# Kernel tuning notes

Measured on AMD Instinct MI355X. Metric: run time of the kernel, lower is better.

The kernel has to match this reference:

```python
import jax, jax.numpy as jnp
import numpy as np

N_NODES = 200000


def _gcn_conv(x, W, b, src, dst, n):
    # PyG GCNConv: h = D^{-1/2} (A + I) D^{-1/2} (x @ W) + b
    h = x @ W  # [N, F_out]
    deg = jax.ops.segment_sum(jnp.ones(dst.shape[0], x.dtype), dst, num_segments=n)
    dinv = jnp.where(deg > 0, jax.lax.rsqrt(deg), 0.0)  # deg_inv_sqrt, inf -> 0
    norm = dinv[src] * dinv[dst]  # [E+N]
    msg = h[src] * norm[:, None]  # gather + scale, dominant memory traffic
    out = jax.ops.segment_sum(msg, dst, num_segments=n)
    return out + b


def setup_inputs() -> dict:
    key = jax.random.key(0)
    k1, k2, k3, k4, k5, k6 = jax.random.split(key, 6)
    x = jax.random.normal(k1, (N_NODES, 1), dtype=jnp.float32)
    edge_index = jax.random.randint(k2, (2, 12800000), 0, N_NODES, dtype=jnp.int64)
    # Glorot-style init like PyG GCNConv
    W1 = jax.random.normal(k3, (1, 16), dtype=jnp.float32) * (1.0 / np.sqrt(1))
    b1 = jnp.zeros((16,), dtype=jnp.float32)
    W2 = jax.random.normal(k4, (16, 1), dtype=jnp.float32) * (1.0 / np.sqrt(16))
    b2 = jnp.zeros((1,), dtype=jnp.float32)
    return {"x": x, "edge_index": edge_index, "W1": W1, "b1": b1, "W2": W2, "b2": b2}


def reference(x, edge_index, W1, b1, W2, b2):
    n = x.shape[0]
    # add self-loops once (static edge count: E + N)
    loops = jnp.arange(n, dtype=edge_index.dtype)
    src = jnp.concatenate([edge_index[0], loops])
    dst = jnp.concatenate([edge_index[1], loops])
    h = _gcn_conv(x, W1, b1, src, dst, n)
    h = jax.nn.relu(h)
    out = _gcn_conv(h, W2, b2, src, dst, n)
    return out
```

## Files before the change

kernel.cpp:

```cpp
#include <hip/hip_runtime.h>

#define TPB 256
#define BTPB 1024
#define STPB 512
#define LOG_S 13
#define S (1 << LOG_S)
#define RMAX 32
#define CHUNK 8192
#define MAXC 40
#define SLACK 32768
#define SCALEF 2097152.0f
#define INV_SCALEF (1.0f / 2097152.0f)


__global__ void k_initcur(int* __restrict__ cur, int R, int cap) {
    int t = threadIdx.x;
    if (t < R) cur[t] = t * cap;
}

__global__ __launch_bounds__(BTPB) void k_bin(const int* __restrict__ dst,
                                              const int* __restrict__ src, int e,
                                              int R, int cap,
                                              int* __restrict__ cur,
                                              unsigned* __restrict__ bkt) {
    __shared__ unsigned stage[CHUNK];
    __shared__ int h[RMAX], lofs[RMAX + 1], gbase[RMAX];
    int t = threadIdx.x;
    int b0 = blockIdx.x * CHUNK;
    int m = min(CHUNK, e - b0);
    if (t < RMAX) h[t] = 0;
    __syncthreads();
    unsigned pack[8];
    int rr[8];
    const int4* d4p = (const int4*)(dst + b0);
    const int4* s4p = (const int4*)(src + b0);
    int m4 = m >> 2;
    #pragma unroll
    for (int g = 0; g < 2; g++) {
        int i4 = g * BTPB + t;
        if (i4 < m4) {
            int4 d = d4p[i4];
            int4 s = s4p[i4];
            #pragma unroll
            for (int k = 0; k < 4; k++) {
                int dd = (k == 0) ? d.x : (k == 1) ? d.y : (k == 2) ? d.z : d.w;
                int ss = (k == 0) ? s.x : (k == 1) ? s.y : (k == 2) ? s.z : s.w;
                int r = dd >> LOG_S;
                pack[g * 4 + k] = ((unsigned)(dd - (r << LOG_S)) << 18) | (unsigned)ss;
                int rk = atomicAdd(&h[r], 1);
                rr[g * 4 + k] = (r << 13) | rk;
            }
        } else {
            #pragma unroll
            for (int k = 0; k < 4; k++) rr[g * 4 + k] = -1;
        }
    }
    __syncthreads();
    if (t < 64) {
        int hv = (t < R) ? h[t] : 0;
        int v = hv;
        for (int o = 1; o < 64; o <<= 1) {
            int u = __shfl_up(v, o);
            if (t >= o) v += u;
        }
        if (t < R) lofs[t] = v - hv;
        if (t == R - 1) lofs[R] = v;
        if (t < R && hv > 0) gbase[t] = atomicAdd(&cur[t], hv);
    }
    __syncthreads();
    #pragma unroll
    for (int k = 0; k < 8; k++) {
        if (rr[k] >= 0)
            stage[lofs[rr[k] >> 13] + (rr[k] & 8191)] = pack[k];
    }
    __syncthreads();
    for (int j = t; j < m; j += BTPB) {
        int lo = 0, hi = R;
        while (hi - lo > 1) {
            int mid = (lo + hi) >> 1;
            if (lofs[mid] <= j) lo = mid; else hi = mid;
        }
        int gi = gbase[lo] + (j - lofs[lo]);
        if (gi < (lo + 1) * cap)
            bkt[gi] = stage[j];
    }
}

template <int MODE>
__global__ __launch_bounds__(STPB) void k_scat(const unsigned* __restrict__ bkt,
                                               const int* __restrict__ cur,
                                               int cap,
                                               const float* __restrict__ val,
                                               int* __restrict__ partials, int bpr) {
    __shared__ int acc[S];
    int t = threadIdx.x;
    int r = blockIdx.x / bpr;
    int c = blockIdx.x - r * bpr;
    int4* acc4 = (int4*)acc;
    for (int j = t; j < S / 4; j += STPB) acc4[j] = make_int4(0, 0, 0, 0);
    __syncthreads();
    const unsigned* bk = bkt + (size_t)r * cap;
    int len = min(cur[r] - r * cap, cap);
    int len4 = len >> 2;
    const uint4* bk4 = (const uint4*)bk;
    int stride = bpr * STPB;
    int i = c * STPB + t;
    if (i < len4) {
        uint4 p = bk4[i];
        for (;;) {
            int inext = i + stride;
            uint4 pn;
            bool hn = inext < len4;
            if (hn) pn = bk4[inext];
            if (MODE == 0) {
                atomicAdd(&acc[p.x >> 18], 1);
                atomicAdd(&acc[p.y >> 18], 1);
                atomicAdd(&acc[p.z >> 18], 1);
                atomicAdd(&acc[p.w >> 18], 1);
            } else {
                atomicAdd(&acc[p.x >> 18], (int)rintf(val[p.x & 0x3FFFFu] * SCALEF));
                atomicAdd(&acc[p.y >> 18], (int)rintf(val[p.y & 0x3FFFFu] * SCALEF));
                atomicAdd(&acc[p.z >> 18], (int)rintf(val[p.z & 0x3FFFFu] * SCALEF));
                atomicAdd(&acc[p.w >> 18], (int)rintf(val[p.w & 0x3FFFFu] * SCALEF));
            }
            if (!hn) break;
            p = pn;
            i = inext;
        }
    }
    for (int k = (len4 << 2) + c * STPB + t; k < len; k += stride) {
        unsigned p = bk[k];
        if (MODE == 0) atomicAdd(&acc[p >> 18], 1);
        else atomicAdd(&acc[p >> 18], (int)rintf(val[p & 0x3FFFFu] * SCALEF));
    }
    __syncthreads();
    int4* out4 = (int4*)(partials + (size_t)blockIdx.x * S);
    for (int j = t; j < S / 4; j += STPB) out4[j] = acc4[j];
}

__device__ inline int redp(const int* __restrict__ partials, int i, int bpr) {
    int r = i >> LOG_S;
    int slot = i & (S - 1);
    const int* p = partials + (size_t)r * bpr * S + slot;
    int s = 0;
    #pragma unroll 8
    for (int c = 0; c < bpr; c++) s += p[(size_t)c * S];
    return s;
}

__global__ void k_red_dinv(const int* __restrict__ partials, int bpr,
                           const float* __restrict__ x, float* __restrict__ dinv,
                           float* __restrict__ y, int n) {
    int i = blockIdx.x * blockDim.x + threadIdx.x;
    if (i < n) {
        float deg = (float)redp(partials, i, bpr) + 1.0f;
        float d = rsqrtf(deg);
        dinv[i] = d;
        y[i] = x[i] * d;
    }
}

__global__ void k_red_node(const int* __restrict__ partials, int bpr,
                           const float* __restrict__ dinv, const float* __restrict__ y,
                           float* __restrict__ z,
                           const float* __restrict__ W1, const float* __restrict__ b1,
                           const float* __restrict__ W2, int n, int f) {
    int i = blockIdx.x * blockDim.x + threadIdx.x;
    if (i < n) {
        float num = (float)redp(partials, i, bpr) * INV_SCALEF;
        float agg = dinv[i] * (num + y[i]);
        float h2 = 0.0f;
        for (int j = 0; j < f; j++) {
            float h = W1[j] * agg + b1[j];
            h2 += fmaxf(h, 0.0f) * W2[j];
        }
        z[i] = h2 * dinv[i];
    }
}

__global__ void k_red_out(const int* __restrict__ partials, int bpr,
                          const float* __restrict__ dinv, const float* __restrict__ z,
                          const float* __restrict__ b2, float* __restrict__ out, int n) {
    int i = blockIdx.x * blockDim.x + threadIdx.x;
    if (i < n) {
        float num = (float)redp(partials, i, bpr) * INV_SCALEF;
        out[i] = dinv[i] * (num + z[i]) + b2[0];
    }
}

__global__ void g_init(float* __restrict__ deg, float* __restrict__ num, int n) {
    int i = blockIdx.x * blockDim.x + threadIdx.x;
    if (i < n) { deg[i] = 1.0f; num[i] = 0.0f; }
}
__global__ void g_deg(const int* __restrict__ dst, float* __restrict__ deg, int e) {
    int i = blockIdx.x * blockDim.x + threadIdx.x;
    if (i < e) atomicAdd(deg + dst[i], 1.0f);
}
__global__ void g_dinv(const float* __restrict__ x, float* __restrict__ dd,
                       float* __restrict__ y, int n) {
    int i = blockIdx.x * blockDim.x + threadIdx.x;
    if (i < n) { float d = rsqrtf(dd[i]); dd[i] = d; y[i] = x[i] * d; }
}
__global__ void g_scatter(const int* __restrict__ src, const int* __restrict__ dst,
                          const float* __restrict__ val, float* __restrict__ num, int e) {
    int i = blockIdx.x * blockDim.x + threadIdx.x;
    if (i < e) atomicAdd(num + dst[i], val[src[i]]);
}
__global__ void g_node(const float* __restrict__ dinv, const float* __restrict__ y,
                       float* __restrict__ num, float* __restrict__ z,
                       const float* __restrict__ W1, const float* __restrict__ b1,
                       const float* __restrict__ W2, int n, int f) {
    int i = blockIdx.x * blockDim.x + threadIdx.x;
    if (i < n) {
        float agg = dinv[i] * (num[i] + y[i]);
        float h2 = 0.0f;
        for (int j = 0; j < f; j++) {
            float h = W1[j] * agg + b1[j];
            h2 += fmaxf(h, 0.0f) * W2[j];
        }
        z[i] = h2 * dinv[i];
        num[i] = 0.0f;
    }
}
__global__ void g_out(const float* __restrict__ dinv, const float* __restrict__ z,
                      const float* __restrict__ num, const float* __restrict__ b2,
                      float* __restrict__ out, int n) {
    int i = blockIdx.x * blockDim.x + threadIdx.x;
    if (i < n) out[i] = dinv[i] * (num[i] + z[i]) + b2[0];
}

extern "C" void kernel_launch(void* const* d_in, const int* in_sizes, int n_in,
                              void* d_out, int out_size, void* d_ws, size_t ws_size,
                              hipStream_t stream) {
    const float* x  = (const float*)d_in[0];
    const int*   ei = (const int*)d_in[1];
    const float* W1 = (const float*)d_in[2];
    const float* b1 = (const float*)d_in[3];
    const float* W2 = (const float*)d_in[4];
    const float* b2 = (const float*)d_in[5];

    int n = in_sizes[0];
    int e = in_sizes[1] / 2;
    int f = in_sizes[2];

    const int* src = ei;
    const int* dst = ei + e;
    float* out = (float*)d_out;

    int R  = (n + S - 1) >> LOG_S;
    int gn = (n + TPB - 1) / TPB;
    size_t words = ws_size / 4;

    size_t o_A   = 0;
    size_t o_B   = o_A + n;
    size_t o_D   = o_B + n;
    size_t o_cur = o_D + n;
    size_t o_bkt = (o_cur + RMAX + 3) & ~(size_t)3;
    int cap = ((e / R) + SLACK + 3) & ~3;
    size_t bkt_w = (size_t)R * cap;
    size_t o_part = o_bkt + bkt_w;

    float* A = (float*)d_ws + o_A;
    float* B = (float*)d_ws + o_B;
    float* D = (float*)d_ws + o_D;
    int*   cur = (int*)d_ws + o_cur;

    int bpr = 0;
    if (R <= RMAX && n <= (1 << 18) && words > o_part) {
        size_t per_c = (size_t)R * S;
        size_t m = (words - o_part) / per_c;
        bpr = (int)(m > MAXC ? MAXC : m);
        while (bpr > 0 && R * bpr > 1024) bpr--;
    }

    if (bpr >= 4) {
        unsigned* bkt = (unsigned*)d_ws + o_bkt;
        int* partials = (int*)d_ws + o_part;
        int gs = R * bpr;
        int gbin = (e + CHUNK - 1) / CHUNK;
        k_initcur<<<1, RMAX, 0, stream>>>(cur, R, cap);
        k_bin<<<gbin, BTPB, 0, stream>>>(dst, src, e, R, cap, cur, bkt);
        k_scat<0><<<gs, STPB, 0, stream>>>(bkt, cur, cap, nullptr, partials, bpr);
        k_red_dinv<<<gn, TPB, 0, stream>>>(partials, bpr, x, A, B, n);
        k_scat<1><<<gs, STPB, 0, stream>>>(bkt, cur, cap, B, partials, bpr);
        k_red_node<<<gn, TPB, 0, stream>>>(partials, bpr, A, B, D, W1, b1, W2, n, f);
        k_scat<1><<<gs, STPB, 0, stream>>>(bkt, cur, cap, D, partials, bpr);
        k_red_out<<<gn, TPB, 0, stream>>>(partials, bpr, A, D, b2, out, n);
    } else {
        float* C = D + n;
        int ge = (e + TPB - 1) / TPB;
        g_init<<<gn, TPB, 0, stream>>>(A, C, n);
        g_deg<<<ge, TPB, 0, stream>>>(dst, A, e);
        g_dinv<<<gn, TPB, 0, stream>>>(x, A, B, n);
        g_scatter<<<ge, TPB, 0, stream>>>(src, dst, B, C, e);
        g_node<<<gn, TPB, 0, stream>>>(A, B, C, D, W1, b1, W2, n, f);
        g_scatter<<<ge, TPB, 0, stream>>>(src, dst, D, C, e);
        g_out<<<gn, TPB, 0, stream>>>(A, D, C, b2, out, n);
    }
}
```

Baseline: 330.9 us.

## Pack degree partials to 16-bit, vectorize reductions, deepen scatter prefetch

The degree-count scatter now writes its per-block histograms as packed 16-bit values, halving partial-buffer traffic for the degree reduction, which reads two nodes per 32-bit word. The node and output reduction kernels each handle four nodes per thread with int4/float4 loads. The scatter loop prefetches two bucket entries ahead and gathers the next entry's values before issuing atomics, to hide gather latency. Packing to 16 bits assumes no per-block count for a node exceeds 65535.

```diff
diff --git a/kernel.cpp b/kernel.cpp
--- a/kernel.cpp
+++ b/kernel.cpp
@@ -104,29 +104,38 @@
     int len4 = len >> 2;
     const uint4* bk4 = (const uint4*)bk;
     int stride = bpr * STPB;
-    int i = c * STPB + t;
-    if (i < len4) {
-        uint4 p = bk4[i];
-        for (;;) {
-            int inext = i + stride;
-            uint4 pn;
-            bool hn = inext < len4;
-            if (hn) pn = bk4[inext];
-            if (MODE == 0) {
-                atomicAdd(&acc[p.x >> 18], 1);
-                atomicAdd(&acc[p.y >> 18], 1);
-                atomicAdd(&acc[p.z >> 18], 1);
-                atomicAdd(&acc[p.w >> 18], 1);
-            } else {
-                atomicAdd(&acc[p.x >> 18], (int)rintf(val[p.x & 0x3FFFFu] * SCALEF));
-                atomicAdd(&acc[p.y >> 18], (int)rintf(val[p.y & 0x3FFFFu] * SCALEF));
-                atomicAdd(&acc[p.z >> 18], (int)rintf(val[p.z & 0x3FFFFu] * SCALEF));
-                atomicAdd(&acc[p.w >> 18], (int)rintf(val[p.w & 0x3FFFFu] * SCALEF));
-            }
-            if (!hn) break;
-            p = pn;
-            i = inext;
-        }
+    int i0 = c * STPB + t;
+    bool h0 = i0 < len4, h1 = (i0 + stride) < len4;
+    uint4 p0, p1;
+    if (h0) p0 = bk4[i0];
+    if (h1) p1 = bk4[i0 + stride];
+    int v0x = 1, v0y = 1, v0z = 1, v0w = 1;
+    if (MODE == 1 && h0) {
+        v0x = (int)rintf(val[p0.x & 0x3FFFFu] * SCALEF);
+        v0y = (int)rintf(val[p0.y & 0x3FFFFu] * SCALEF);
+        v0z = (int)rintf(val[p0.z & 0x3FFFFu] * SCALEF);
+        v0w = (int)rintf(val[p0.w & 0x3FFFFu] * SCALEF);
+    }
+    int inext = i0 + 2 * stride;
+    while (h0) {
+        uint4 p2;
+        bool h2 = inext < len4;
+        if (h2) p2 = bk4[inext];
+        int v1x = 1, v1y = 1, v1z = 1, v1w = 1;
+        if (MODE == 1 && h1) {
+            v1x = (int)rintf(val[p1.x & 0x3FFFFu] * SCALEF);
+            v1y = (int)rintf(val[p1.y & 0x3FFFFu] * SCALEF);
+            v1z = (int)rintf(val[p1.z & 0x3FFFFu] * SCALEF);
+            v1w = (int)rintf(val[p1.w & 0x3FFFFu] * SCALEF);
+        }
+        atomicAdd(&acc[p0.x >> 18], v0x);
+        atomicAdd(&acc[p0.y >> 18], v0y);
+        atomicAdd(&acc[p0.z >> 18], v0z);
+        atomicAdd(&acc[p0.w >> 18], v0w);
+        p0 = p1; h0 = h1;
+        p1 = p2; h1 = h2;
+        v0x = v1x; v0y = v1y; v0z = v1z; v0w = v1w;
+        inext += stride;
     }
     for (int k = (len4 << 2) + c * STPB + t; k < len; k += stride) {
         unsigned p = bk[k];
@@ -134,11 +143,20 @@
         else atomicAdd(&acc[p >> 18], (int)rintf(val[p & 0x3FFFFu] * SCALEF));
     }
     __syncthreads();
-    int4* out4 = (int4*)(partials + (size_t)blockIdx.x * S);
-    for (int j = t; j < S / 4; j += STPB) out4[j] = acc4[j];
-}
-
-__device__ inline int redp(const int* __restrict__ partials, int i, int bpr) {
+    if (MODE == 0) {
+        unsigned* o16 = (unsigned*)((unsigned short*)partials + (size_t)blockIdx.x * S);
+        const int2* acc2 = (const int2*)acc;
+        for (int j = t; j < S / 2; j += STPB) {
+            int2 a = acc2[j];
+            o16[j] = (unsigned)a.x | ((unsigned)a.y << 16);
+        }
+    } else {
+        int4* out4 = (int4*)(partials + (size_t)blockIdx.x * S);
+        for (int j = t; j < S / 4; j += STPB) out4[j] = acc4[j];
+    }
+}
+
+__device__ __forceinline__ int redp(const int* __restrict__ partials, int i, int bpr) {
     int r = i >> LOG_S;
     int slot = i & (S - 1);
     const int* p = partials + (size_t)r * bpr * S + slot;
@@ -151,12 +169,35 @@
 __global__ void k_red_dinv(const int* __restrict__ partials, int bpr,
                            const float* __restrict__ x, float* __restrict__ dinv,
                            float* __restrict__ y, int n) {
-    int i = blockIdx.x * blockDim.x + threadIdx.x;
-    if (i < n) {
-        float deg = (float)redp(partials, i, bpr) + 1.0f;
-        float d = rsqrtf(deg);
-        dinv[i] = d;
-        y[i] = x[i] * d;
+    int i2 = blockIdx.x * blockDim.x + threadIdx.x;
+    int i = i2 << 1;
+    if (i + 1 < n) {
+        int r = i >> LOG_S;
+        int slot = i & (S - 1);
+        const unsigned* pb = (const unsigned*)partials
+                             + (size_t)r * bpr * (S / 2) + (slot >> 1);
+        int s0 = 0, s1 = 0;
+        #pragma unroll 8
+        for (int c = 0; c < bpr; c++) {
+            unsigned v = pb[(size_t)c * (S / 2)];
+            s0 += (int)(v & 0xFFFFu);
+            s1 += (int)(v >> 16);
+        }
+        float d0 = rsqrtf((float)s0 + 1.0f);
+        float d1 = rsqrtf((float)s1 + 1.0f);
+        float2 xx = *(const float2*)(x + i);
+        *(float2*)(dinv + i) = make_float2(d0, d1);
+        *(float2*)(y + i) = make_float2(xx.x * d0, xx.y * d1);
+    } else if (i < n) {
+        int r = i >> LOG_S;
+        int slot = i & (S - 1);
+        const unsigned short* pb = (const unsigned short*)partials
+                                   + (size_t)r * bpr * S + slot;
+        int s0 = 0;
+        for (int c = 0; c < bpr; c++) s0 += (int)pb[(size_t)c * S];
+        float d0 = rsqrtf((float)s0 + 1.0f);
+        dinv[i] = d0;
+        y[i] = x[i] * d0;
     }
 }
 
@@ -165,26 +206,76 @@
                            float* __restrict__ z,
                            const float* __restrict__ W1, const float* __restrict__ b1,
                            const float* __restrict__ W2, int n, int f) {
-    int i = blockIdx.x * blockDim.x + threadIdx.x;
-    if (i < n) {
-        float num = (float)redp(partials, i, bpr) * INV_SCALEF;
-        float agg = dinv[i] * (num + y[i]);
-        float h2 = 0.0f;
+    int q = blockIdx.x * blockDim.x + threadIdx.x;
+    int i = q << 2;
+    if (i + 3 < n) {
+        int r = i >> LOG_S;
+        int slot = i & (S - 1);
+        const int4* p = (const int4*)(partials + (size_t)r * bpr * S + slot);
+        int4 s = make_int4(0, 0, 0, 0);
+        #pragma unroll 8
+        for (int c = 0; c < bpr; c++) {
+            int4 v = p[(size_t)c * (S / 4)];
+            s.x += v.x; s.y += v.y; s.z += v.z; s.w += v.w;
+        }
+        float4 dv = *(const float4*)(dinv + i);
+        float4 yy = *(const float4*)(y + i);
+        float a0 = dv.x * ((float)s.x * INV_SCALEF + yy.x);
+        float a1 = dv.y * ((float)s.y * INV_SCALEF + yy.y);
+        float a2 = dv.z * ((float)s.z * INV_SCALEF + yy.z);
+        float a3 = dv.w * ((float)s.w * INV_SCALEF + yy.w);
+        float c0 = 0.0f, c1 = 0.0f, c2 = 0.0f, c3 = 0.0f;
         for (int j = 0; j < f; j++) {
-            float h = W1[j] * agg + b1[j];
-            h2 += fmaxf(h, 0.0f) * W2[j];
-        }
-        z[i] = h2 * dinv[i];
+            float w = W1[j], bb = b1[j], u = W2[j];
+            c0 += fmaxf(w * a0 + bb, 0.0f) * u;
+            c1 += fmaxf(w * a1 + bb, 0.0f) * u;
+            c2 += fmaxf(w * a2 + bb, 0.0f) * u;
+            c3 += fmaxf(w * a3 + bb, 0.0f) * u;
+        }
+        *(float4*)(z + i) = make_float4(c0 * dv.x, c1 * dv.y, c2 * dv.z, c3 * dv.w);
+    } else {
+        for (int k = i; k < n && k < i + 4; k++) {
+            float num = (float)redp(partials, k, bpr) * INV_SCALEF;
+            float agg = dinv[k] * (num + y[k]);
+            float h2 = 0.0f;
+            for (int j = 0; j < f; j++) {
+                float h = W1[j] * agg + b1[j];
+                h2 += fmaxf(h, 0.0f) * W2[j];
+            }
+            z[k] = h2 * dinv[k];
+        }
     }
 }
 
 __global__ void k_red_out(const int* __restrict__ partials, int bpr,
                           const float* __restrict__ dinv, const float* __restrict__ z,
                           const float* __restrict__ b2, float* __restrict__ out, int n) {
-    int i = blockIdx.x * blockDim.x + threadIdx.x;
-    if (i < n) {
-        float num = (float)redp(partials, i, bpr) * INV_SCALEF;
-        out[i] = dinv[i] * (num + z[i]) + b2[0];
+    int q = blockIdx.x * blockDim.x + threadIdx.x;
+    int i = q << 2;
+    if (i + 3 < n) {
+        int r = i >> LOG_S;
+        int slot = i & (S - 1);
+        const int4* p = (const int4*)(partials + (size_t)r * bpr * S + slot);
+        int4 s = make_int4(0, 0, 0, 0);
+        #pragma unroll 8
+        for (int c = 0; c < bpr; c++) {
+            int4 v = p[(size_t)c * (S / 4)];
+            s.x += v.x; s.y += v.y; s.z += v.z; s.w += v.w;
+        }
+        float4 dv = *(const float4*)(dinv + i);
+        float4 zz = *(const float4*)(z + i);
+        float bb = b2[0];
+        float4 o;
+        o.x = dv.x * ((float)s.x * INV_SCALEF + zz.x) + bb;
+        o.y = dv.y * ((float)s.y * INV_SCALEF + zz.y) + bb;
+        o.z = dv.z * ((float)s.z * INV_SCALEF + zz.z) + bb;
+        o.w = dv.w * ((float)s.w * INV_SCALEF + zz.w) + bb;
+        *(float4*)(out + i) = o;
+    } else {
+        for (int k = i; k < n && k < i + 4; k++) {
+            float num = (float)redp(partials, k, bpr) * INV_SCALEF;
+            out[k] = dinv[k] * (num + z[k]) + b2[0];
+        }
     }
 }
 
@@ -278,14 +369,16 @@
         int* partials = (int*)d_ws + o_part;
         int gs = R * bpr;
         int gbin = (e + CHUNK - 1) / CHUNK;
+        int gn2 = (((n + 1) >> 1) + TPB - 1) / TPB;
+        int gn4 = (((n + 3) >> 2) + TPB - 1) / TPB;
         k_initcur<<<1, RMAX, 0, stream>>>(cur, R, cap);
         k_bin<<<gbin, BTPB, 0, stream>>>(dst, src, e, R, cap, cur, bkt);
         k_scat<0><<<gs, STPB, 0, stream>>>(bkt, cur, cap, nullptr, partials, bpr);
-        k_red_dinv<<<gn, TPB, 0, stream>>>(partials, bpr, x, A, B, n);
+        k_red_dinv<<<gn2, TPB, 0, stream>>>(partials, bpr, x, A, B, n);
         k_scat<1><<<gs, STPB, 0, stream>>>(bkt, cur, cap, B, partials, bpr);
-        k_red_node<<<gn, TPB, 0, stream>>>(partials, bpr, A, B, D, W1, b1, W2, n, f);
+        k_red_node<<<gn4, TPB, 0, stream>>>(partials, bpr, A, B, D, W1, b1, W2, n, f);
         k_scat<1><<<gs, STPB, 0, stream>>>(bkt, cur, cap, D, partials, bpr);
-        k_red_out<<<gn, TPB, 0, stream>>>(partials, bpr, A, D, b2, out, n);
+        k_red_out<<<gn4, TPB, 0, stream>>>(partials, bpr, A, D, b2, out, n);
     } else {
         float* C = D + n;
         int ge = (e + TPB - 1) / TPB;
```

Measured after the change: 328.6 us. About the same (-0.7%).
